# Kernel tuning notes

Measured on AMD Instinct MI355X. Metric: run time of the kernel, lower is better.

## Reference

```python
import jax, jax.numpy as jnp
import numpy as np

B, S, D = 8, 1024, 768
H, HD = 12, 64  # heads, head dim (H*HD == D)
EPS = 1e-12


def setup_inputs() -> dict:
    key = jax.random.key(0)
    ks = jax.random.split(key, 8)
    s = 0.02
    return {
        "hidden_states": jax.random.normal(ks[0], (B, S, D), jnp.float32),
        "attention_mask": jnp.zeros((B, 1, 1, S), jnp.float32),
        "head_mask": jnp.ones((H,), jnp.float32),
        "Wq": jax.random.normal(ks[1], (D, H * HD), jnp.float32) * s,
        "bq": jnp.zeros((H * HD,), jnp.float32),
        "Wk": jax.random.normal(ks[2], (D, H * HD), jnp.float32) * s,
        "bk": jnp.zeros((H * HD,), jnp.float32),
        "Wv": jax.random.normal(ks[3], (D, H * HD), jnp.float32) * s,
        "bv": jnp.zeros((H * HD,), jnp.float32),
        "Wo": jax.random.normal(ks[4], (D, H * HD), jnp.float32) * s,  # torch Linear weight [out=D, in=H*HD]
        "bo": jnp.zeros((D,), jnp.float32),
        "gamma": jnp.ones((D,), jnp.float32),
        "beta": jnp.zeros((D,), jnp.float32),
    }


def reference(hidden_states, attention_mask, head_mask, Wq, bq, Wk, bk, Wv, bv, Wo, bo, gamma, beta):
    def heads(x):  # [B,S,H*HD] -> [B,H,S,HD]
        return x.reshape(B, S, H, HD).transpose(0, 2, 1, 3)

    q = heads(hidden_states @ Wq.T + bq)
    k = heads(hidden_states @ Wk.T + bk)
    v = heads(hidden_states @ Wv.T + bv)

    scores = jnp.einsum("bhqd,bhkd->bhqk", q, k) / np.sqrt(HD).astype(np.float32)
    scores = scores + attention_mask
    probs = jax.nn.softmax(scores, axis=-1)  # dropout p=0 (eval)
    ctx = jnp.einsum("bhqk,bhkd->bhqd", probs, v)  # [B,H,S,HD]

    # masked per-head output projection: Wo.T.view(H, HD, D)
    Wph = Wo.T.reshape(H, HD, D)
    proj = jnp.einsum("bhsd,hde,h->bse", ctx, Wph, head_mask) + bo

    # residual + LayerNorm
    x = proj + hidden_states
    mu = jnp.mean(x, axis=-1, keepdims=True)
    var = jnp.mean(jnp.square(x - mu), axis=-1, keepdims=True)
    out = (x - mu) * jax.lax.rsqrt(var + EPS) * gamma + beta
    return out
```

## Files before the change

### kernel.cpp

```cpp
#include <hip/hip_runtime.h>
#include <hip/hip_bf16.h>
#include <math.h>

#define Bn 8
#define Sn 1024
#define Dn 768
#define Hn 12
#define MROWS (Bn * Sn)

typedef __attribute__((ext_vector_type(8))) short short8;
typedef __attribute__((ext_vector_type(4))) float floatx4;

__device__ __forceinline__ unsigned short f2b(float x) {
    union { float f; unsigned u; } v; v.f = x;
    unsigned r = v.u + 0x7fffu + ((v.u >> 16) & 1u);
    return (unsigned short)(r >> 16);
}

__device__ __forceinline__ unsigned pk2(float a, float b) {
    union { __hip_bfloat162 h; unsigned u; } v;
    v.h = __float22bfloat162_rn(float2{a, b});
    return v.u;
}

__device__ __forceinline__ float fexp2(float x) {
    float r;
    asm("v_exp_f32 %0, %1" : "=v"(r) : "v"(x));
    return r;
}

__device__ __forceinline__ void gload16(const void* g, void* l) {
    __builtin_amdgcn_global_load_lds(
        (const __attribute__((address_space(1))) void*)g,
        (__attribute__((address_space(3))) void*)l, 16, 0, 0);
}

#define MEMFENCE() asm volatile("" ::: "memory")
#define WAITV8()  asm volatile("s_waitcnt vmcnt(8)" ::: "memory")
#define WAITV6()  asm volatile("s_waitcnt vmcnt(6)" ::: "memory")
#define WAITV4()  asm volatile("s_waitcnt vmcnt(4)" ::: "memory")
#define WAITV0()  asm volatile("s_waitcnt vmcnt(0)" ::: "memory")
#define WAITLGKM() asm volatile("s_waitcnt lgkmcnt(0)" ::: "memory")

__global__ __launch_bounds__(256) void convert_all(const float* __restrict__ X,
                                                   const float* __restrict__ Wq, const float* __restrict__ Wk,
                                                   const float* __restrict__ Wv, const float* __restrict__ Wo,
                                                   unsigned short* __restrict__ Xb,
                                                   unsigned short* __restrict__ Wqb, unsigned short* __restrict__ Wkb,
                                                   unsigned short* __restrict__ Wvb, unsigned short* __restrict__ Wob) {
    const int id = blockIdx.x;
    const float* src;
    unsigned short* dst;
    int i;
    if (id < 6144) {
        src = X; dst = Xb;
        i = id * 256 + threadIdx.x;
    } else {
        const int y = (id - 6144) / 576;
        src = (y == 0) ? Wq : (y == 1) ? Wk : (y == 2) ? Wv : Wo;
        dst = (y == 0) ? Wqb : (y == 1) ? Wkb : (y == 2) ? Wvb : Wob;
        i = ((id - 6144) % 576) * 256 + threadIdx.x;
    }
    float4 v = reinterpret_cast<const float4*>(src)[i];
    ushort4 o;
    o.x = f2b(v.x); o.y = f2b(v.y); o.z = f2b(v.z); o.w = f2b(v.w);
    reinterpret_cast<ushort4*>(dst)[i] = o;
}

#define QKV_STAGE(t, b)                                                        \
    {                                                                          \
        const int k0 = (t) * 32;                                               \
        gload16(gAsrc[0] + k0, lAdst[0] + (b) * 4096);                         \
        gload16(gAsrc[1] + k0, lAdst[1] + (b) * 4096);                         \
        gload16(gWsrc[0] + k0, lWdst[0] + (b) * 4096);                         \
        gload16(gWsrc[1] + k0, lWdst[1] + (b) * 4096);                         \
    }

#define QKV_COMP(b)                                                            \
    {                                                                          \
        const unsigned short* Ab = &As[b][0];                                  \
        const unsigned short* Wb = &Ws[b][0];                                  \
        short8 bf[4];                                                          \
        _Pragma("unroll") for (int j = 0; j < 4; j++)                          \
            bf[j] = *(const short8*)&Wb[woff[j]];                              \
        __builtin_amdgcn_s_setprio(1);                                         \
        _Pragma("unroll") for (int i = 0; i < 4; i++) {                        \
            short8 af = *(const short8*)&Ab[aoff[i]];                          \
            _Pragma("unroll") for (int j = 0; j < 4; j++)                      \
                acc[i][j] = __builtin_amdgcn_mfma_f32_16x16x32_bf16(           \
                    af, bf[j], acc[i][j], 0, 0, 0);                            \
        }                                                                      \
        __builtin_amdgcn_s_setprio(0);                                         \
    }

__global__ __launch_bounds__(256, 3) void gemm_qkv(const unsigned short* __restrict__ A,
                                                   const unsigned short* __restrict__ Wq,
                                                   const unsigned short* __restrict__ Wk,
                                                   const unsigned short* __restrict__ Wv,
                                                   const float* __restrict__ bq,
                                                   const float* __restrict__ bk,
                                                   const float* __restrict__ bv,
                                                   unsigned short* __restrict__ Qh,
                                                   unsigned short* __restrict__ Kh,
                                                   unsigned short* __restrict__ Vt) {
    __shared__ __align__(16) unsigned short As[3][128 * 32];
    __shared__ __align__(16) unsigned short Ws[3][128 * 32];
    const int id = blockIdx.x;
    const int by = id & 63;
    const int bx = id >> 6;
    const int mat = bx / 6;
    const int m0 = by * 128;
    const int n0 = (bx % 6) * 128;
    const unsigned short* W = (mat == 0) ? Wq : (mat == 1) ? Wk : Wv;
    const float* bias = (mat == 0) ? bq : (mat == 1) ? bk : bv;
    unsigned short* Cout = (mat == 0) ? Qh : (mat == 1) ? Kh : Vt;

    const int tid = threadIdx.x;
    const int w = tid >> 6, l = tid & 63, quad = l >> 4, mr = l & 15;
    const int wm = (w >> 1) * 64, wn = (w & 1) * 64;

    const unsigned short* gAsrc[2];
    const unsigned short* gWsrc[2];
    unsigned short* lAdst[2];
    unsigned short* lWdst[2];
#pragma unroll
    for (int j = 0; j < 2; j++) {
        const int u = tid + j * 256;
        const int r = u >> 2, c = u & 3;
        const int cp = c ^ ((r >> 1) & 3);
        gAsrc[j] = &A[(size_t)(m0 + r) * Dn + cp * 8];
        gWsrc[j] = &W[(size_t)(n0 + r) * Dn + cp * 8];
        lAdst[j] = &As[0][u * 8];
        lWdst[j] = &Ws[0][u * 8];
    }

    int aoff[4], woff[4];
#pragma unroll
    for (int i = 0; i < 4; i++) {
        const int ra = wm + i * 16 + mr;
        aoff[i] = (ra * 4 + (quad ^ ((ra >> 1) & 3))) * 8;
    }
#pragma unroll
    for (int j = 0; j < 4; j++) {
        const int rw = wn + j * 16 + mr;
        woff[j] = (rw * 4 + (quad ^ ((rw >> 1) & 3))) * 8;
    }

    floatx4 acc[4][4];
#pragma unroll
    for (int i = 0; i < 4; i++)
#pragma unroll
        for (int j = 0; j < 4; j++) {
            floatx4 z = {0.f, 0.f, 0.f, 0.f};
            acc[i][j] = z;
        }

    QKV_STAGE(0, 0);
    QKV_STAGE(1, 1);

    for (int t = 0; t < 21; t += 3) {
        WAITV4();
        __builtin_amdgcn_s_barrier();
        MEMFENCE();
        QKV_STAGE(t + 2, 2);
        QKV_COMP(0);

        WAITV4();
        __builtin_amdgcn_s_barrier();
        MEMFENCE();
        QKV_STAGE(t + 3, 0);
        QKV_COMP(1);

        WAITV4();
        __builtin_amdgcn_s_barrier();
        MEMFENCE();
        QKV_STAGE(t + 4, 1);
        QKV_COMP(2);
    }
    WAITV4();
    __builtin_amdgcn_s_barrier();
    MEMFENCE();
    QKV_STAGE(23, 2);
    QKV_COMP(0);

    WAITV4();
    __builtin_amdgcn_s_barrier();
    MEMFENCE();
    QKV_COMP(1);

    WAITV0();
    __builtin_amdgcn_s_barrier();
    MEMFENCE();
    QKV_COMP(2);

#pragma unroll
    for (int j = 0; j < 4; j++) {
        const int col = n0 + wn + j * 16 + mr;
        const float bval = bias[col];
        const int h = col >> 6, d = col & 63;
#pragma unroll
        for (int i = 0; i < 4; i++) {
            const int mbase = m0 + wm + i * 16 + quad * 4;
            const int b = mbase >> 10, s0 = mbase & 1023;
            const size_t base = (size_t)(b * Hn + h) << 16;
            if (mat == 2) {
                ushort4 o;
                o.x = f2b(acc[i][j][0] + bval);
                o.y = f2b(acc[i][j][1] + bval);
                o.z = f2b(acc[i][j][2] + bval);
                o.w = f2b(acc[i][j][3] + bval);
                *reinterpret_cast<ushort4*>(&Cout[base + (size_t)d * 1024 + s0]) = o;
            } else {
#pragma unroll
                for (int r = 0; r < 4; r++) {
                    const float val = acc[i][j][r] + bval;
                    Cout[base + (size_t)(s0 + r) * 64 + d] = f2b(val);
                }
            }
        }
    }
}

#define OUT_COMPUTE(Ab, Wb)                                                    \
    {                                                                          \
        short8 af[4][2], bf[2][2];                                             \
        _Pragma("unroll") for (int i = 0; i < 4; i++)                          \
            _Pragma("unroll") for (int ks = 0; ks < 2; ks++)                   \
                af[i][ks] = *(const short8*)&(Ab)[aoff[i][ks]];                \
        _Pragma("unroll") for (int j = 0; j < 2; j++)                          \
            _Pragma("unroll") for (int ks = 0; ks < 2; ks++)                   \
                bf[j][ks] = *(const short8*)&(Wb)[woff[j][ks]];                \
        __builtin_amdgcn_s_setprio(1);                                         \
        _Pragma("unroll") for (int ks = 0; ks < 2; ks++)                       \
            _Pragma("unroll") for (int i = 0; i < 4; i++)                      \
                _Pragma("unroll") for (int j = 0; j < 2; j++)                  \
                    acc[i][j] = __builtin_amdgcn_mfma_f32_16x16x32_bf16(       \
                        af[i][ks], bf[j][ks], acc[i][j], 0, 0, 0);             \
        __builtin_amdgcn_s_setprio(0);                                         \
    }

__global__ __launch_bounds__(256) void gemm_out(const unsigned short* __restrict__ A,
                                                const unsigned short* __restrict__ W,
                                                const float* __restrict__ bias,
                                                const float* __restrict__ X,
                                                float* __restrict__ xres) {
    __shared__ __align__(16) unsigned short As[2][64 * 64];
    __shared__ __align__(16) unsigned short Ws[2][128 * 64];
    const int id = blockIdx.x;
    const int by = id & 127;
    const int bx = id >> 7;
    const int m0 = by * 64;
    const int n0 = bx * 128;

    const int tid = threadIdx.x;
    const int w = tid >> 6, l = tid & 63, quad = l >> 4, mr = l & 15;

    const unsigned short* gAsrc[2];
    unsigned short* lAdst[2];
#pragma unroll
    for (int j = 0; j < 2; j++) {
        const int u = tid + j * 256;
        const int r = u >> 3, c = u & 7;
        gAsrc[j] = &A[(size_t)(m0 + r) * Dn + (c ^ (r & 7)) * 8];
        lAdst[j] = &As[0][u * 8];
    }
    const unsigned short* gWsrc[4];
    unsigned short* lWdst[4];
#pragma unroll
    for (int j = 0; j < 4; j++) {
        const int u = tid + j * 256;
        const int r = u >> 3, c = u & 7;
        gWsrc[j] = &W[(size_t)(n0 + r) * Dn + (c ^ (r & 7)) * 8];
        lWdst[j] = &Ws[0][u * 8];
    }

    int aoff[4][2], woff[2][2];
#pragma unroll
    for (int i = 0; i < 4; i++) {
        const int ra = i * 16 + mr;
#pragma unroll
        for (int ks = 0; ks < 2; ks++)
            aoff[i][ks] = (ra * 8 + ((quad + ks * 4) ^ (ra & 7))) * 8;
    }
#pragma unroll
    for (int j = 0; j < 2; j++) {
        const int rw = w * 32 + j * 16 + mr;
#pragma unroll
        for (int ks = 0; ks < 2; ks++)
            woff[j][ks] = (rw * 8 + ((quad + ks * 4) ^ (rw & 7))) * 8;
    }

    floatx4 acc[4][2];
#pragma unroll
    for (int i = 0; i < 4; i++)
#pragma unroll
        for (int j = 0; j < 2; j++) {
            floatx4 z = {0.f, 0.f, 0.f, 0.f};
            acc[i][j] = z;
        }

    const unsigned short* Af = &As[0][0];
    const unsigned short* Wf = &Ws[0][0];

#pragma unroll
    for (int j = 0; j < 2; j++) gload16(gAsrc[j], lAdst[j]);
#pragma unroll
    for (int j = 0; j < 4; j++) gload16(gWsrc[j], lWdst[j]);

    for (int kt = 0; kt < 12; kt += 2) {
        {
            const int k0 = (kt + 1) * 64;
#pragma unroll
            for (int j = 0; j < 2; j++) gload16(gAsrc[j] + k0, lAdst[j] + 4096);
#pragma unroll
            for (int j = 0; j < 4; j++) gload16(gWsrc[j] + k0, lWdst[j] + 8192);
        }
        WAITV6();
        __builtin_amdgcn_s_barrier();
        MEMFENCE();
        OUT_COMPUTE(Af, Wf);
        __builtin_amdgcn_s_barrier();
        MEMFENCE();

        if (kt + 2 < 12) {
            const int k0 = (kt + 2) * 64;
#pragma unroll
            for (int j = 0; j < 2; j++) gload16(gAsrc[j] + k0, lAdst[j]);
#pragma unroll
            for (int j = 0; j < 4; j++) gload16(gWsrc[j] + k0, lWdst[j]);
            WAITV6();
        } else {
            WAITV0();
        }
        __builtin_amdgcn_s_barrier();
        MEMFENCE();
        OUT_COMPUTE(Af + 4096, Wf + 8192);
        __builtin_amdgcn_s_barrier();
        MEMFENCE();
    }

#pragma unroll
    for (int j = 0; j < 2; j++) {
        const int col = n0 + w * 32 + j * 16 + mr;
        const float bval = bias[col];
#pragma unroll
        for (int i = 0; i < 4; i++) {
#pragma unroll
            for (int r = 0; r < 4; r++) {
                const int m = m0 + i * 16 + quad * 4 + r;
                xres[(size_t)m * Dn + col] = acc[i][j][r] + bval + X[(size_t)m * Dn + col];
            }
        }
    }
}

__global__ __launch_bounds__(256) void flash_attn_mfma(const unsigned short* __restrict__ Qh,
                                                       const unsigned short* __restrict__ Kh,
                                                       const unsigned short* __restrict__ Vt,
                                                       const float* __restrict__ mask,
                                                       const float* __restrict__ head_mask,
                                                       unsigned short* __restrict__ ctx) {
    __shared__ __align__(16) unsigned short Ks[64 * 72];
    __shared__ __align__(16) unsigned short Vs[64 * 72];
    __shared__ __align__(16) unsigned short Ps[128 * 72];
    __shared__ float msk[64];

    const float LOG2E = 1.44269504088896f;
    const float C1 = 0.125f * 1.44269504088896f;

    const int id = blockIdx.x;
    const int bh = id % 96;
    const int qt = id / 96;
    const int b = bh / Hn, h = bh % Hn;
    const int q0 = qt * 128;
    const int tid = threadIdx.x;
    const int w = tid >> 6, l = tid & 63, quad = l >> 4, mr = l & 15;
    const size_t hb = (size_t)(b * Hn + h) << 16;

    short8 aq[2][2];
#pragma unroll
    for (int j = 0; j < 2; j++)
#pragma unroll
        for (int ks = 0; ks < 2; ks++)
            aq[j][ks] = *(const short8*)&Qh[hb + (size_t)(q0 + w * 32 + j * 16 + mr) * 64 + ks * 32 + quad * 8];

    float l_s[2] = {0.f, 0.f};
    floatx4 oacc[2][4];
#pragma unroll
    for (int i = 0; i < 2; i++)
#pragma unroll
        for (int jj = 0; jj < 4; jj++) {
            floatx4 z = {0.f, 0.f, 0.f, 0.f};
            oacc[i][jj] = z;
        }

    const int srow = tid >> 2;
    const int scol = (tid & 3) * 16;

    short8 pk0 = *(const short8*)&Kh[hb + (size_t)srow * 64 + scol];
    short8 pk1 = *(const short8*)&Kh[hb + (size_t)srow * 64 + scol + 8];
    short8 pv0 = *(const short8*)&Vt[hb + (size_t)srow * 1024 + scol];
    short8 pv1 = *(const short8*)&Vt[hb + (size_t)srow * 1024 + scol + 8];
    float pm = mask[b * Sn + (tid & 63)];

    for (int kt = 0; kt < Sn / 64; kt++) {
        __builtin_amdgcn_s_barrier();
        MEMFENCE();
        *(short8*)&Ks[srow * 72 + scol] = pk0;
        *(short8*)&Ks[srow * 72 + scol + 8] = pk1;
        *(short8*)&Vs[srow * 72 + scol] = pv0;
        *(short8*)&Vs[srow * 72 + scol + 8] = pv1;
        if (tid < 64) msk[tid] = pm * LOG2E;
        if (kt < Sn / 64 - 1) {
            const int k0 = (kt + 1) * 64;
            pk0 = *(const short8*)&Kh[hb + (size_t)(k0 + srow) * 64 + scol];
            pk1 = *(const short8*)&Kh[hb + (size_t)(k0 + srow) * 64 + scol + 8];
            pv0 = *(const short8*)&Vt[hb + (size_t)srow * 1024 + k0 + scol];
            pv1 = *(const short8*)&Vt[hb + (size_t)srow * 1024 + k0 + scol + 8];
            pm = mask[b * Sn + k0 + (tid & 63)];
        }
        WAITLGKM();
        __builtin_amdgcn_s_barrier();
        MEMFENCE();

        floatx4 sacc[4][2];
#pragma unroll
        for (int i = 0; i < 4; i++)
#pragma unroll
            for (int j = 0; j < 2; j++) {
                floatx4 z = {0.f, 0.f, 0.f, 0.f};
                sacc[i][j] = z;
            }
#pragma unroll
        for (int ks = 0; ks < 2; ks++) {
            short8 kfr[4];
#pragma unroll
            for (int i = 0; i < 4; i++)
                kfr[i] = *(const short8*)&Ks[(i * 16 + mr) * 72 + ks * 32 + quad * 8];
            __builtin_amdgcn_s_setprio(1);
#pragma unroll
            for (int i = 0; i < 4; i++)
#pragma unroll
                for (int j = 0; j < 2; j++)
                    sacc[i][j] = __builtin_amdgcn_mfma_f32_16x16x32_bf16(kfr[i], aq[j][ks], sacc[i][j], 0, 0, 0);
            __builtin_amdgcn_s_setprio(0);
        }

#pragma unroll
        for (int i = 0; i < 4; i++) {
            floatx4 mk4 = *(const floatx4*)&msk[i * 16 + quad * 4];
#pragma unroll
            for (int j = 0; j < 2; j++) {
                float p[4];
#pragma unroll
                for (int r = 0; r < 4; r++) {
                    p[r] = fexp2(sacc[i][j][r] * C1 + mk4[r]);
                    l_s[j] += p[r];
                }
                uint2 w2;
                w2.x = pk2(p[0], p[1]);
                w2.y = pk2(p[2], p[3]);
                *(uint2*)&Ps[(w * 32 + j * 16 + mr) * 72 + i * 16 + quad * 4] = w2;
            }
        }

#pragma unroll
        for (int ks = 0; ks < 2; ks++) {
            short8 ap0 = *(const short8*)&Ps[(w * 32 + mr) * 72 + ks * 32 + quad * 8];
            short8 ap1 = *(const short8*)&Ps[(w * 32 + 16 + mr) * 72 + ks * 32 + quad * 8];
            __builtin_amdgcn_s_setprio(1);
#pragma unroll
            for (int jj = 0; jj < 4; jj++) {
                short8 bv = *(const short8*)&Vs[(jj * 16 + mr) * 72 + ks * 32 + quad * 8];
                oacc[0][jj] = __builtin_amdgcn_mfma_f32_16x16x32_bf16(ap0, bv, oacc[0][jj], 0, 0, 0);
                oacc[1][jj] = __builtin_amdgcn_mfma_f32_16x16x32_bf16(ap1, bv, oacc[1][jj], 0, 0, 0);
            }
            __builtin_amdgcn_s_setprio(0);
        }
    }

    float L[2];
#pragma unroll
    for (int j = 0; j < 2; j++) {
        float t = l_s[j];
        t += __shfl_xor(t, 16);
        t += __shfl_xor(t, 32);
        L[j] = t;
    }
    const float hm = head_mask[h];
    float inv[2][4];
#pragma unroll
    for (int i = 0; i < 2; i++)
#pragma unroll
        for (int r = 0; r < 4; r++)
            inv[i][r] = hm / __shfl(L[i], quad * 4 + r);

#pragma unroll
    for (int i = 0; i < 2; i++)
#pragma unroll
        for (int jj = 0; jj < 4; jj++)
#pragma unroll
            for (int r = 0; r < 4; r++) {
                const int qrow = q0 + w * 32 + i * 16 + quad * 4 + r;
                ctx[(size_t)(b * Sn + qrow) * Dn + h * 64 + jj * 16 + mr] = f2b(oacc[i][jj][r] * inv[i][r]);
            }
}

__global__ __launch_bounds__(256) void ln_kernel(const float* __restrict__ x,
                                                 const float* __restrict__ gamma,
                                                 const float* __restrict__ beta,
                                                 float* __restrict__ out) {
    __shared__ float r1[4];
    __shared__ float r2[4];
    const int m = blockIdx.x;
    const int tid = threadIdx.x;
    const int w = tid >> 6, lane = tid & 63;

    float xv[3];
    float s = 0.f, ss = 0.f;
#pragma unroll
    for (int i = 0; i < 3; i++) {
        int j = tid + i * 256;
        float t = x[(size_t)m * Dn + j];
        xv[i] = t;
        s += t;
        ss += t * t;
    }
#pragma unroll
    for (int o = 1; o < 64; o <<= 1) {
        s += __shfl_xor(s, o);
        ss += __shfl_xor(ss, o);
    }
    if (lane == 0) { r1[w] = s; r2[w] = ss; }
    __syncthreads();
    const float sum = r1[0] + r1[1] + r1[2] + r1[3];
    const float sqs = r2[0] + r2[1] + r2[2] + r2[3];
    const float mu = sum * (1.0f / Dn);
    const float var = sqs * (1.0f / Dn) - mu * mu;
    const float rstd = rsqrtf(var + 1e-12f);
#pragma unroll
    for (int i = 0; i < 3; i++) {
        int j = tid + i * 256;
        out[(size_t)m * Dn + j] = (xv[i] - mu) * rstd * gamma[j] + beta[j];
    }
}

extern "C" void kernel_launch(void* const* d_in, const int* in_sizes, int n_in,
                              void* d_out, int out_size, void* d_ws, size_t ws_size,
                              hipStream_t stream) {
    const float* X         = (const float*)d_in[0];
    const float* mask      = (const float*)d_in[1];
    const float* head_mask = (const float*)d_in[2];
    const float* Wq        = (const float*)d_in[3];
    const float* bq        = (const float*)d_in[4];
    const float* Wk        = (const float*)d_in[5];
    const float* bk        = (const float*)d_in[6];
    const float* Wv        = (const float*)d_in[7];
    const float* bv        = (const float*)d_in[8];
    const float* Wo        = (const float*)d_in[9];
    const float* bo        = (const float*)d_in[10];
    const float* gamma     = (const float*)d_in[11];
    const float* beta      = (const float*)d_in[12];
    float* out = (float*)d_out;

    const size_t NE = (size_t)Bn * Sn * Dn;
    const size_t NW = (size_t)Dn * Dn;

    char* p = (char*)d_ws;
    unsigned short* Xb  = (unsigned short*)p;  p += NE * 2;
    unsigned short* Wqb = (unsigned short*)p;  p += NW * 2;
    unsigned short* Wkb = (unsigned short*)p;  p += NW * 2;
    unsigned short* Wvb = (unsigned short*)p;  p += NW * 2;
    unsigned short* Wob = (unsigned short*)p;  p += NW * 2;
    unsigned short* Qh  = (unsigned short*)p;  p += NE * 2;
    unsigned short* Kh  = (unsigned short*)p;  p += NE * 2;
    unsigned short* Vtb = (unsigned short*)p;  p += NE * 2;
    unsigned short* ctx = (unsigned short*)p;  p += NE * 2;
    float* xres = (float*)p;

    convert_all<<<8448, 256, 0, stream>>>(X, Wq, Wk, Wv, Wo, Xb, Wqb, Wkb, Wvb, Wob);

    gemm_qkv<<<1152, 256, 0, stream>>>(Xb, Wqb, Wkb, Wvb, bq, bk, bv, Qh, Kh, Vtb);

    flash_attn_mfma<<<768, 256, 0, stream>>>(Qh, Kh, Vtb, mask, head_mask, ctx);

    gemm_out<<<768, 256, 0, stream>>>(ctx, Wob, bo, X, xres);

    ln_kernel<<<MROWS, 256, 0, stream>>>(xres, gamma, beta, out);
}
```

Measured before the change: 212.3 us.

## Enlarge QKV GEMM tile to 256 rows with remapped block order, triple-buffer out GEMM

The QKV projection kernel now uses 512-thread blocks computing 256x128 tiles, with a block-index remap that groups blocks sharing the same A rows onto nearby block IDs for cache locality. This halves the block count and lets each W tile feed more rows. The output-projection GEMM moves from a double-buffered K=64 pipeline to a triple-buffered K=32 pipeline matching the QKV kernel's structure. The larger tiles raise LDS and register use per block, which may lower occupancy, and the wait counts must match the new per-stage load count.

After: 220.9 us. +4.0%, slower.

```diff
diff --git a/kernel.cpp b/kernel.cpp
--- a/kernel.cpp
+++ b/kernel.cpp
@@ -36,11 +36,10 @@
 }
 
 #define MEMFENCE() asm volatile("" ::: "memory")
-#define WAITV8()  asm volatile("s_waitcnt vmcnt(8)" ::: "memory")
-#define WAITV6()  asm volatile("s_waitcnt vmcnt(6)" ::: "memory")
-#define WAITV4()  asm volatile("s_waitcnt vmcnt(4)" ::: "memory")
+#define WAITV3()  asm volatile("s_waitcnt vmcnt(3)" ::: "memory")
 #define WAITV0()  asm volatile("s_waitcnt vmcnt(0)" ::: "memory")
 #define WAITLGKM() asm volatile("s_waitcnt lgkmcnt(0)" ::: "memory")
+
 
 __global__ __launch_bounds__(256) void convert_all(const float* __restrict__ X,
                                                    const float* __restrict__ Wq, const float* __restrict__ Wk,
@@ -70,10 +69,9 @@
 #define QKV_STAGE(t, b)                                                        \
     {                                                                          \
         const int k0 = (t) * 32;                                               \
-        gload16(gAsrc[0] + k0, lAdst[0] + (b) * 4096);                         \
-        gload16(gAsrc[1] + k0, lAdst[1] + (b) * 4096);                         \
-        gload16(gWsrc[0] + k0, lWdst[0] + (b) * 4096);                         \
-        gload16(gWsrc[1] + k0, lWdst[1] + (b) * 4096);                         \
+        gload16(gAsrc[0] + k0, lAdst[0] + (b) * 8192);                         \
+        gload16(gAsrc[1] + k0, lAdst[1] + (b) * 8192);                         \
+        gload16(gWsrc + k0, lWdst + (b) * 4096);                               \
     }
 
 #define QKV_COMP(b)                                                            \
@@ -93,7 +91,7 @@
         __builtin_amdgcn_s_setprio(0);                                         \
     }
 
-__global__ __launch_bounds__(256, 3) void gemm_qkv(const unsigned short* __restrict__ A,
+__global__ __launch_bounds__(512, 4) void gemm_qkv(const unsigned short* __restrict__ A,
                                                    const unsigned short* __restrict__ Wq,
                                                    const unsigned short* __restrict__ Wk,
                                                    const unsigned short* __restrict__ Wv,
@@ -103,35 +101,43 @@
                                                    unsigned short* __restrict__ Qh,
                                                    unsigned short* __restrict__ Kh,
                                                    unsigned short* __restrict__ Vt) {
-    __shared__ __align__(16) unsigned short As[3][128 * 32];
+    __shared__ __align__(16) unsigned short As[3][256 * 32];
     __shared__ __align__(16) unsigned short Ws[3][128 * 32];
-    const int id = blockIdx.x;
-    const int by = id & 63;
-    const int bx = id >> 6;
-    const int mat = bx / 6;
-    const int m0 = by * 128;
-    const int n0 = (bx % 6) * 128;
+    const int orig = blockIdx.x;
+    const int chunk = orig & 7;
+    const int local = orig >> 3;
+    const int by = chunk * 4 + local / 18;
+    const int bxr = local % 18;
+    const int mat = bxr / 6;
+    const int m0 = by * 256;
+    const int n0 = (bxr % 6) * 128;
     const unsigned short* W = (mat == 0) ? Wq : (mat == 1) ? Wk : Wv;
     const float* bias = (mat == 0) ? bq : (mat == 1) ? bk : bv;
     unsigned short* Cout = (mat == 0) ? Qh : (mat == 1) ? Kh : Vt;
 
     const int tid = threadIdx.x;
     const int w = tid >> 6, l = tid & 63, quad = l >> 4, mr = l & 15;
-    const int wm = (w >> 1) * 64, wn = (w & 1) * 64;
+    const int wm = (w >> 1) * 64;
+    const int wn = (w & 1) * 64;
 
     const unsigned short* gAsrc[2];
-    const unsigned short* gWsrc[2];
     unsigned short* lAdst[2];
-    unsigned short* lWdst[2];
 #pragma unroll
     for (int j = 0; j < 2; j++) {
-        const int u = tid + j * 256;
+        const int u = tid + j * 512;
         const int r = u >> 2, c = u & 3;
         const int cp = c ^ ((r >> 1) & 3);
         gAsrc[j] = &A[(size_t)(m0 + r) * Dn + cp * 8];
-        gWsrc[j] = &W[(size_t)(n0 + r) * Dn + cp * 8];
         lAdst[j] = &As[0][u * 8];
-        lWdst[j] = &Ws[0][u * 8];
+    }
+    const unsigned short* gWsrc;
+    unsigned short* lWdst;
+    {
+        const int u = tid;
+        const int r = u >> 2, c = u & 3;
+        const int cp = c ^ ((r >> 1) & 3);
+        gWsrc = &W[(size_t)(n0 + r) * Dn + cp * 8];
+        lWdst = &Ws[0][u * 8];
     }
 
     int aoff[4], woff[4];
@@ -159,31 +165,31 @@
     QKV_STAGE(1, 1);
 
     for (int t = 0; t < 21; t += 3) {
-        WAITV4();
+        WAITV3();
         __builtin_amdgcn_s_barrier();
         MEMFENCE();
         QKV_STAGE(t + 2, 2);
         QKV_COMP(0);
 
-        WAITV4();
+        WAITV3();
         __builtin_amdgcn_s_barrier();
         MEMFENCE();
         QKV_STAGE(t + 3, 0);
         QKV_COMP(1);
 
-        WAITV4();
+        WAITV3();
         __builtin_amdgcn_s_barrier();
         MEMFENCE();
         QKV_STAGE(t + 4, 1);
         QKV_COMP(2);
     }
-    WAITV4();
+    WAITV3();
     __builtin_amdgcn_s_barrier();
     MEMFENCE();
     QKV_STAGE(23, 2);
     QKV_COMP(0);
 
-    WAITV4();
+    WAITV3();
     __builtin_amdgcn_s_barrier();
     MEMFENCE();
     QKV_COMP(1);
@@ -221,31 +227,38 @@
     }
 }
 
-#define OUT_COMPUTE(Ab, Wb)                                                    \
+#define OUT_STAGE(t, b)                                                        \
     {                                                                          \
-        short8 af[4][2], bf[2][2];                                             \
-        _Pragma("unroll") for (int i = 0; i < 4; i++)                          \
-            _Pragma("unroll") for (int ks = 0; ks < 2; ks++)                   \
-                af[i][ks] = *(const short8*)&(Ab)[aoff[i][ks]];                \
+        const int k0 = (t) * 32;                                               \
+        gload16(gAsrc + k0, lAdst + (b) * 2048);                               \
+        gload16(gWsrc[0] + k0, lWdst[0] + (b) * 4096);                         \
+        gload16(gWsrc[1] + k0, lWdst[1] + (b) * 4096);                         \
+    }
+
+#define OUT_COMP(b)                                                            \
+    {                                                                          \
+        const unsigned short* Ab = &As[b][0];                                  \
+        const unsigned short* Wb = &Ws[b][0];                                  \
+        short8 bf[2];                                                          \
         _Pragma("unroll") for (int j = 0; j < 2; j++)                          \
-            _Pragma("unroll") for (int ks = 0; ks < 2; ks++)                   \
-                bf[j][ks] = *(const short8*)&(Wb)[woff[j][ks]];                \
+            bf[j] = *(const short8*)&Wb[woff[j]];                              \
         __builtin_amdgcn_s_setprio(1);                                         \
-        _Pragma("unroll") for (int ks = 0; ks < 2; ks++)                       \
-            _Pragma("unroll") for (int i = 0; i < 4; i++)                      \
-                _Pragma("unroll") for (int j = 0; j < 2; j++)                  \
-                    acc[i][j] = __builtin_amdgcn_mfma_f32_16x16x32_bf16(       \
-                        af[i][ks], bf[j][ks], acc[i][j], 0, 0, 0);             \
+        _Pragma("unroll") for (int i = 0; i < 4; i++) {                        \
+            short8 af = *(const short8*)&Ab[aoff[i]];                          \
+            _Pragma("unroll") for (int j = 0; j < 2; j++)                      \
+                acc[i][j] = __builtin_amdgcn_mfma_f32_16x16x32_bf16(           \
+                    af, bf[j], acc[i][j], 0, 0, 0);                            \
+        }                                                                      \
         __builtin_amdgcn_s_setprio(0);                                         \
     }
 
-__global__ __launch_bounds__(256) void gemm_out(const unsigned short* __restrict__ A,
-                                                const unsigned short* __restrict__ W,
-                                                const float* __restrict__ bias,
-                                                const float* __restrict__ X,
-                                                float* __restrict__ xres) {
-    __shared__ __align__(16) unsigned short As[2][64 * 64];
-    __shared__ __align__(16) unsigned short Ws[2][128 * 64];
+__global__ __launch_bounds__(256, 4) void gemm_out(const unsigned short* __restrict__ A,
+                                                   const unsigned short* __restrict__ W,
+                                                   const float* __restrict__ bias,
+                                                   const float* __restrict__ X,
+                                                   float* __restrict__ xres) {
+    __shared__ __align__(16) unsigned short As[3][64 * 32];
+    __shared__ __align__(16) unsigned short Ws[3][128 * 32];
     const int id = blockIdx.x;
     const int by = id & 127;
     const int bx = id >> 7;
@@ -255,39 +268,36 @@
     const int tid = threadIdx.x;
     const int w = tid >> 6, l = tid & 63, quad = l >> 4, mr = l & 15;
 
-    const unsigned short* gAsrc[2];
-    unsigned short* lAdst[2];
+    const unsigned short* gAsrc;
+    unsigned short* lAdst;
+    {
+        const int u = tid;
+        const int r = u >> 2, c = u & 3;
+        const int cp = c ^ ((r >> 1) & 3);
+        gAsrc = &A[(size_t)(m0 + r) * Dn + cp * 8];
+        lAdst = &As[0][u * 8];
+    }
+    const unsigned short* gWsrc[2];
+    unsigned short* lWdst[2];
 #pragma unroll
     for (int j = 0; j < 2; j++) {
         const int u = tid + j * 256;
-        const int r = u >> 3, c = u & 7;
-        gAsrc[j] = &A[(size_t)(m0 + r) * Dn + (c ^ (r & 7)) * 8];
-        lAdst[j] = &As[0][u * 8];
-    }
-    const unsigned short* gWsrc[4];
-    unsigned short* lWdst[4];
-#pragma unroll
-    for (int j = 0; j < 4; j++) {
-        const int u = tid + j * 256;
-        const int r = u >> 3, c = u & 7;
-        gWsrc[j] = &W[(size_t)(n0 + r) * Dn + (c ^ (r & 7)) * 8];
+        const int r = u >> 2, c = u & 3;
+        const int cp = c ^ ((r >> 1) & 3);
+        gWsrc[j] = &W[(size_t)(n0 + r) * Dn + cp * 8];
         lWdst[j] = &Ws[0][u * 8];
     }
 
-    int aoff[4][2], woff[2][2];
+    int aoff[4], woff[2];
 #pragma unroll
     for (int i = 0; i < 4; i++) {
         const int ra = i * 16 + mr;
-#pragma unroll
-        for (int ks = 0; ks < 2; ks++)
-            aoff[i][ks] = (ra * 8 + ((quad + ks * 4) ^ (ra & 7))) * 8;
+        aoff[i] = (ra * 4 + (quad ^ ((ra >> 1) & 3))) * 8;
     }
 #pragma unroll
     for (int j = 0; j < 2; j++) {
         const int rw = w * 32 + j * 16 + mr;
-#pragma unroll
-        for (int ks = 0; ks < 2; ks++)
-            woff[j][ks] = (rw * 8 + ((quad + ks * 4) ^ (rw & 7))) * 8;
+        woff[j] = (rw * 4 + (quad ^ ((rw >> 1) & 3))) * 8;
     }
 
     floatx4 acc[4][2];
@@ -299,45 +309,43 @@
             acc[i][j] = z;
         }
 
-    const unsigned short* Af = &As[0][0];
-    const unsigned short* Wf = &Ws[0][0];
-
-#pragma unroll
-    for (int j = 0; j < 2; j++) gload16(gAsrc[j], lAdst[j]);
-#pragma unroll
-    for (int j = 0; j < 4; j++) gload16(gWsrc[j], lWdst[j]);
-
-    for (int kt = 0; kt < 12; kt += 2) {
-        {
-            const int k0 = (kt + 1) * 64;
-#pragma unroll
-            for (int j = 0; j < 2; j++) gload16(gAsrc[j] + k0, lAdst[j] + 4096);
-#pragma unroll
-            for (int j = 0; j < 4; j++) gload16(gWsrc[j] + k0, lWdst[j] + 8192);
-        }
-        WAITV6();
-        __builtin_amdgcn_s_barrier();
-        MEMFENCE();
-        OUT_COMPUTE(Af, Wf);
-        __builtin_amdgcn_s_barrier();
-        MEMFENCE();
-
-        if (kt + 2 < 12) {
-            const int k0 = (kt + 2) * 64;
-#pragma unroll
-            for (int j = 0; j < 2; j++) gload16(gAsrc[j] + k0, lAdst[j]);
-#pragma unroll
-            for (int j = 0; j < 4; j++) gload16(gWsrc[j] + k0, lWdst[j]);
-            WAITV6();
-        } else {
-            WAITV0();
-        }
-        __builtin_amdgcn_s_barrier();
-        MEMFENCE();
-        OUT_COMPUTE(Af + 4096, Wf + 8192);
-        __builtin_amdgcn_s_barrier();
-        MEMFENCE();
-    }
+    OUT_STAGE(0, 0);
+    OUT_STAGE(1, 1);
+
+    for (int t = 0; t < 21; t += 3) {
+        WAITV3();
+        __builtin_amdgcn_s_barrier();
+        MEMFENCE();
+        OUT_STAGE(t + 2, 2);
+        OUT_COMP(0);
+
+        WAITV3();
+        __builtin_amdgcn_s_barrier();
+        MEMFENCE();
+        OUT_STAGE(t + 3, 0);
+        OUT_COMP(1);
+
+        WAITV3();
+        __builtin_amdgcn_s_barrier();
+        MEMFENCE();
+        OUT_STAGE(t + 4, 1);
+        OUT_COMP(2);
+    }
+    WAITV3();
+    __builtin_amdgcn_s_barrier();
+    MEMFENCE();
+    OUT_STAGE(23, 2);
+    OUT_COMP(0);
+
+    WAITV3();
+    __builtin_amdgcn_s_barrier();
+    MEMFENCE();
+    OUT_COMP(1);
+
+    WAITV0();
+    __builtin_amdgcn_s_barrier();
+    MEMFENCE();
+    OUT_COMP(2);
 
 #pragma unroll
     for (int j = 0; j < 2; j++) {
@@ -580,7 +588,7 @@
 
     convert_all<<<8448, 256, 0, stream>>>(X, Wq, Wk, Wv, Wo, Xb, Wqb, Wkb, Wvb, Wob);
 
-    gemm_qkv<<<1152, 256, 0, stream>>>(Xb, Wqb, Wkb, Wvb, bq, bk, bv, Qh, Kh, Vtb);
+    gemm_qkv<<<576, 512, 0, stream>>>(Xb, Wqb, Wkb, Wvb, bq, bk, bv, Qh, Kh, Vtb);
 
     flash_attn_mfma<<<768, 256, 0, stream>>>(Qh, Kh, Vtb, mask, head_mask, ctx);
 
```

## Load V fragments and mask directly from global into registers in flash attention

Applied to the files above, without the earlier changes.

Drops the LDS staging buffers for V and the mask in the attention kernel. Each wave now reads its V^T MFMA fragments and its mask values straight from global memory, issued before the softmax so the latency can hide behind the exp work. This removes LDS stores and reads plus the register prefetch of V, and frees shared memory that may allow more resident blocks. In exchange, all four waves load the same V tile redundantly from global memory or cache, and V is no longer prefetched a full iteration ahead.

Measured after the change: 250.1 us. 1.18x slower.

```diff
diff --git a/kernel.cpp b/kernel.cpp
--- a/kernel.cpp
+++ b/kernel.cpp
@@ -36,7 +36,6 @@
 }
 
 #define MEMFENCE() asm volatile("" ::: "memory")
-#define WAITV8()  asm volatile("s_waitcnt vmcnt(8)" ::: "memory")
 #define WAITV6()  asm volatile("s_waitcnt vmcnt(6)" ::: "memory")
 #define WAITV4()  asm volatile("s_waitcnt vmcnt(4)" ::: "memory")
 #define WAITV0()  asm volatile("s_waitcnt vmcnt(0)" ::: "memory")
@@ -361,9 +360,7 @@
                                                        const float* __restrict__ head_mask,
                                                        unsigned short* __restrict__ ctx) {
     __shared__ __align__(16) unsigned short Ks[64 * 72];
-    __shared__ __align__(16) unsigned short Vs[64 * 72];
     __shared__ __align__(16) unsigned short Ps[128 * 72];
-    __shared__ float msk[64];
 
     const float LOG2E = 1.44269504088896f;
     const float C1 = 0.125f * 1.44269504088896f;
@@ -399,25 +396,22 @@
 
     short8 pk0 = *(const short8*)&Kh[hb + (size_t)srow * 64 + scol];
     short8 pk1 = *(const short8*)&Kh[hb + (size_t)srow * 64 + scol + 8];
-    short8 pv0 = *(const short8*)&Vt[hb + (size_t)srow * 1024 + scol];
-    short8 pv1 = *(const short8*)&Vt[hb + (size_t)srow * 1024 + scol + 8];
-    float pm = mask[b * Sn + (tid & 63)];
 
     for (int kt = 0; kt < Sn / 64; kt++) {
+        const int k0 = kt * 64;
         __builtin_amdgcn_s_barrier();
         MEMFENCE();
         *(short8*)&Ks[srow * 72 + scol] = pk0;
         *(short8*)&Ks[srow * 72 + scol + 8] = pk1;
-        *(short8*)&Vs[srow * 72 + scol] = pv0;
-        *(short8*)&Vs[srow * 72 + scol + 8] = pv1;
-        if (tid < 64) msk[tid] = pm * LOG2E;
         if (kt < Sn / 64 - 1) {
-            const int k0 = (kt + 1) * 64;
-            pk0 = *(const short8*)&Kh[hb + (size_t)(k0 + srow) * 64 + scol];
-            pk1 = *(const short8*)&Kh[hb + (size_t)(k0 + srow) * 64 + scol + 8];
-            pv0 = *(const short8*)&Vt[hb + (size_t)srow * 1024 + k0 + scol];
-            pv1 = *(const short8*)&Vt[hb + (size_t)srow * 1024 + k0 + scol + 8];
-            pm = mask[b * Sn + k0 + (tid & 63)];
+            pk0 = *(const short8*)&Kh[hb + (size_t)(k0 + 64 + srow) * 64 + scol];
+            pk1 = *(const short8*)&Kh[hb + (size_t)(k0 + 64 + srow) * 64 + scol + 8];
+        }
+        floatx4 mkv[4];
+#pragma unroll
+        for (int i = 0; i < 4; i++) {
+            floatx4 t = *(const floatx4*)&mask[b * Sn + k0 + i * 16 + quad * 4];
+            mkv[i] = t * LOG2E;
         }
         WAITLGKM();
         __builtin_amdgcn_s_barrier();
@@ -446,15 +440,21 @@
             __builtin_amdgcn_s_setprio(0);
         }
 
+        short8 bvv[2][4];
+#pragma unroll
+        for (int ks = 0; ks < 2; ks++)
+#pragma unroll
+            for (int jj = 0; jj < 4; jj++)
+                bvv[ks][jj] = *(const short8*)&Vt[hb + (size_t)(jj * 16 + mr) * 1024 + k0 + ks * 32 + quad * 8];
+
 #pragma unroll
         for (int i = 0; i < 4; i++) {
-            floatx4 mk4 = *(const floatx4*)&msk[i * 16 + quad * 4];
 #pragma unroll
             for (int j = 0; j < 2; j++) {
                 float p[4];
 #pragma unroll
                 for (int r = 0; r < 4; r++) {
-                    p[r] = fexp2(sacc[i][j][r] * C1 + mk4[r]);
+                    p[r] = fexp2(sacc[i][j][r] * C1 + mkv[i][r]);
                     l_s[j] += p[r];
                 }
                 uint2 w2;
@@ -471,9 +471,8 @@
             __builtin_amdgcn_s_setprio(1);
 #pragma unroll
             for (int jj = 0; jj < 4; jj++) {
-                short8 bv = *(const short8*)&Vs[(jj * 16 + mr) * 72 + ks * 32 + quad * 8];
-                oacc[0][jj] = __builtin_amdgcn_mfma_f32_16x16x32_bf16(ap0, bv, oacc[0][jj], 0, 0, 0);
-                oacc[1][jj] = __builtin_amdgcn_mfma_f32_16x16x32_bf16(ap1, bv, oacc[1][jj], 0, 0, 0);
+                oacc[0][jj] = __builtin_amdgcn_mfma_f32_16x16x32_bf16(ap0, bvv[ks][jj], oacc[0][jj], 0, 0, 0);
+                oacc[1][jj] = __builtin_amdgcn_mfma_f32_16x16x32_bf16(ap1, bvv[ks][jj], oacc[1][jj], 0, 0, 0);
             }
             __builtin_amdgcn_s_setprio(0);
         }
```
